# Kernel optimization log

Measured on AMD Instinct MI355X. Metric: run time of the kernel, lower is better.

Reference implementation:

```python
import jax, jax.numpy as jnp
import numpy as np

D_MODEL = 1024
N_LAYERS = 4
D_INNER = 2 * D_MODEL          # expand=2
D_STATE = 16
D_CONV = 4
DT_RANK = D_MODEL // 16        # ceil(1024/16)=64
B, T = 2, 1024


def setup_inputs() -> dict:
    key = jax.random.key(0)
    ks = jax.random.split(key, 8)
    s = 0.02
    return {
        "x": jax.random.normal(ks[0], (B, T, D_MODEL), jnp.float32),
        "in_proj_w": jax.random.normal(ks[1], (N_LAYERS, 2 * D_INNER, D_MODEL), jnp.float32) * s,
        "conv_w": jax.random.normal(ks[2], (N_LAYERS, D_INNER, D_CONV), jnp.float32) * s,
        "conv_b": jnp.zeros((N_LAYERS, D_INNER), jnp.float32),
        "x_proj_w": jax.random.normal(ks[3], (N_LAYERS, DT_RANK + 2 * D_STATE, D_INNER), jnp.float32) * s,
        "dt_proj_w": jax.random.normal(ks[4], (N_LAYERS, D_INNER, DT_RANK), jnp.float32) * s,
        "dt_proj_b": jax.random.normal(ks[5], (N_LAYERS, D_INNER), jnp.float32) * 0.1,
        "A_log": jnp.tile(jnp.log(jnp.arange(1.0, D_STATE + 1.0, dtype=jnp.float32)), (N_LAYERS, D_INNER, 1)),
        "Dd": jnp.ones((N_LAYERS, D_INNER), jnp.float32),
        "out_proj_w": jax.random.normal(ks[6], (N_LAYERS, D_MODEL, D_INNER), jnp.float32) * s,
        "norm_w": jnp.ones((D_MODEL,), jnp.float32),
        "norm_b": jnp.zeros((D_MODEL,), jnp.float32),
    }


def _silu(v):
    return v * jax.nn.sigmoid(v)


def _mamba_block(x, in_w, cw, cb, xp_w, dtp_w, dtp_b, A_log, Dv, out_w):
    # x: [B,T,d_model]
    xz = jnp.einsum('btd,ed->bte', x, in_w)            # [B,T,2*d_inner]
    u, z = jnp.split(xz, 2, axis=-1)                   # each [B,T,d_inner]
    # causal depthwise conv over time
    uc = jax.lax.conv_general_dilated(
        u.transpose(0, 2, 1),                          # [B,d_inner,T]
        cw[:, None, :],                                # [d_inner,1,K]
        window_strides=(1,), padding=[(D_CONV - 1, 0)],
        feature_group_count=D_INNER,
        dimension_numbers=('NCH', 'OIH', 'NCH'))
    uc = _silu(uc.transpose(0, 2, 1) + cb)             # [B,T,d_inner]
    x_dbl = jnp.einsum('btd,ed->bte', uc, xp_w)        # [B,T,dt_rank+2*d_state]
    dt_r = x_dbl[..., :DT_RANK]
    Bm = x_dbl[..., DT_RANK:DT_RANK + D_STATE]         # [B,T,d_state]
    Cm = x_dbl[..., DT_RANK + D_STATE:]                # [B,T,d_state]
    dt = jax.nn.softplus(jnp.einsum('btr,dr->btd', dt_r, dtp_w) + dtp_b)  # [B,T,d_inner]
    A = -jnp.exp(A_log)                                # [d_inner,d_state]

    def step(h, inp):
        u_t, dt_t, B_t, C_t = inp                      # [B,dI],[B,dI],[B,dS],[B,dS]
        h = jnp.exp(dt_t[..., None] * A) * h + (dt_t * u_t)[..., None] * B_t[:, None, :]
        return h, jnp.einsum('bds,bs->bd', h, C_t)

    h0 = jnp.zeros((x.shape[0], D_INNER, D_STATE), x.dtype)
    xs = (uc.transpose(1, 0, 2), dt.transpose(1, 0, 2), Bm.transpose(1, 0, 2), Cm.transpose(1, 0, 2))
    _, ys = jax.lax.scan(step, h0, xs)                 # ys: [T,B,d_inner]
    y = ys.transpose(1, 0, 2) + uc * Dv                # skip term D*u
    y = y * _silu(z)                                   # gated
    return jnp.einsum('btd,ed->bte', y, out_w)         # [B,T,d_model]


def reference(x, in_proj_w, conv_w, conv_b, x_proj_w, dt_proj_w, dt_proj_b, A_log, Dd, out_proj_w, norm_w, norm_b):
    for i in range(in_proj_w.shape[0]):
        residual = x
        x = _mamba_block(x, in_proj_w[i], conv_w[i], conv_b[i], x_proj_w[i],
                         dt_proj_w[i], dt_proj_b[i], A_log[i], Dd[i], out_proj_w[i])
        x = x + residual
    mu = jnp.mean(x, -1, keepdims=True)
    var = jnp.var(x, -1, keepdims=True)
    return (x - mu) / jnp.sqrt(var + 1e-5) * norm_w + norm_b
```

## Files before the change

kernel.cpp:

```cpp
#include <hip/hip_runtime.h>
#include <hip/hip_bf16.h>

#define N_LAYERS 4
#define D_MODEL  1024
#define D_INNER  2048
#define D_STATE  16
#define D_CONV   4
#define DT_RANK  64
#define BB       2
#define TT       1024
#define BT       (BB*TT)

#define NCHUNK 32
#define SCTC   (TT/NCHUNK)

#define XP_KS  8

typedef unsigned short ushort_t;
typedef __attribute__((ext_vector_type(8))) short short8;
typedef __attribute__((ext_vector_type(4))) float f32x4;

__device__ __forceinline__ float sigmoidf_(float x){ return 1.f/(1.f+__expf(-x)); }
__device__ __forceinline__ float siluf_(float x){ return x*sigmoidf_(x); }
__device__ __forceinline__ float softplusf_(float x){ return fmaxf(x,0.f) + log1pf(__expf(-fabsf(x))); }
__device__ __forceinline__ ushort_t f2b(float f){
    unsigned int x = __builtin_bit_cast(unsigned int, f);
    unsigned int r = (x + 0x7fffu + ((x>>16)&1u)) >> 16;
    return (ushort_t)r;
}
__device__ __forceinline__ float b2f(ushort_t u){
    unsigned int x = ((unsigned int)u) << 16;
    return __builtin_bit_cast(float, x);
}

#define GLOAD(g, l) __builtin_amdgcn_global_load_lds( \
    (const __attribute__((address_space(1))) void*)(g), \
    (__attribute__((address_space(3))) void*)(l), 16, 0, 0)

__global__ __launch_bounds__(256) void f2b_k(const float* __restrict__ in,
                                             ushort_t* __restrict__ out, int n){
    int i = blockIdx.x*256 + threadIdx.x;
    float4 v = ((const float4*)in)[i];
    ushort4 o;
    o.x = f2b(v.x); o.y = f2b(v.y); o.z = f2b(v.z); o.w = f2b(v.w);
    ((ushort4*)out)[i] = o;
}

__global__ __launch_bounds__(256) void f2bw_k(
    const float* __restrict__ in_w, const float* __restrict__ out_w,
    const float* __restrict__ dtp_w,
    ushort_t* __restrict__ winb, ushort_t* __restrict__ woutb,
    ushort_t* __restrict__ dtpb){
    const int n1 = (N_LAYERS*4096*1024)/4;
    const int n2 = (N_LAYERS*1024*2048)/4;
    int i = blockIdx.x*256 + threadIdx.x;
    const float4* src; ushort4* dst; int j;
    if (i < n1){ src=(const float4*)in_w;  dst=(ushort4*)winb;  j=i; }
    else if (i < n1+n2){ src=(const float4*)out_w; dst=(ushort4*)woutb; j=i-n1; }
    else { src=(const float4*)dtp_w; dst=(ushort4*)dtpb; j=i-n1-n2; }
    float4 v = src[j];
    ushort4 o;
    o.x = f2b(v.x); o.y = f2b(v.y); o.z = f2b(v.z); o.w = f2b(v.w);
    dst[j] = o;
}

__global__ __launch_bounds__(512) void gemm_ip(
    const ushort_t* __restrict__ A, const ushort_t* __restrict__ W,
    int M, int N, int K, ushort_t* __restrict__ outb,
    int RM, int RN, int XN)
{
    __shared__ ushort_t As[4][128*32];
    __shared__ ushort_t Ws[4][128*32];
    const int tid  = threadIdx.x;
    const int lane = tid & 63;
    const int wv   = tid >> 6;
    const int wm0  = (wv>>2)*64, wn0 = (wv&3)*32;

    const int bid = blockIdx.x;
    const int xcd = bid & 7, bi = bid >> 3;
    const int xm = xcd / XN, xn = xcd - xm*XN;
    const int m0 = (xm*RM + bi/RN)*128;
    const int n0 = (xn*RN + bi - (bi/RN)*RN)*128;

    const int r0 = tid>>2, ch = tid&3;

    f32x4 acc[4][2];
    #pragma unroll
    for (int i=0;i<4;++i)
        #pragma unroll
        for (int j=0;j<2;++j) acc[i][j] = (f32x4){0.f,0.f,0.f,0.f};

    const int row_a = lane & 15, kc = (lane>>4)*8;
    const ushort_t* gA = A + (size_t)(m0+r0)*K + ch*8;
    const ushort_t* gW = W + (size_t)(n0+r0)*K + ch*8;

#define STAGE(KT, BUF) { \
    GLOAD(gA + (KT)*32, (char*)&As[BUF][0] + tid*16); \
    GLOAD(gW + (KT)*32, (char*)&Ws[BUF][0] + tid*16); }

#define COMPUTE(BUF) { \
    short8 af[4], bf[2]; \
    _Pragma("unroll") \
    for (int i=0;i<4;++i) af[i] = *(const short8*)&As[BUF][(wm0 + i*16 + row_a)*32 + kc]; \
    _Pragma("unroll") \
    for (int j=0;j<2;++j) bf[j] = *(const short8*)&Ws[BUF][(wn0 + j*16 + row_a)*32 + kc]; \
    _Pragma("unroll") \
    for (int i=0;i<4;++i) \
        _Pragma("unroll") \
        for (int j=0;j<2;++j) \
            acc[i][j] = __builtin_amdgcn_mfma_f32_16x16x32_bf16(af[i], bf[j], acc[i][j], 0,0,0); }

    const int nt = K >> 5;
    STAGE(0, 0); STAGE(1, 1); STAGE(2, 2);
    for (int t = 0; t < nt-3; ++t){
        asm volatile("s_waitcnt vmcnt(4)" ::: "memory");
        asm volatile("s_barrier" ::: "memory");
        STAGE(t+3, (t+3)&3);
        COMPUTE(t&3);
    }
    asm volatile("s_waitcnt vmcnt(4)" ::: "memory");
    asm volatile("s_barrier" ::: "memory");
    COMPUTE((nt-3)&3);
    asm volatile("s_waitcnt vmcnt(2)" ::: "memory");
    asm volatile("s_barrier" ::: "memory");
    COMPUTE((nt-2)&3);
    asm volatile("s_waitcnt vmcnt(0)" ::: "memory");
    asm volatile("s_barrier" ::: "memory");
    COMPUTE((nt-1)&3);
#undef STAGE
#undef COMPUTE

    const int crow = (lane>>4)*4, ccol = lane & 15;
    #pragma unroll
    for (int i=0;i<4;++i){
        #pragma unroll
        for (int j=0;j<2;++j){
            #pragma unroll
            for (int r=0;r<4;++r){
                int m = m0 + wm0 + i*16 + crow + r;
                int n = n0 + wn0 + j*16 + ccol;
                outb[(size_t)m*N + n] = f2b(acc[i][j][r]);
            }
        }
    }
}

__global__ __launch_bounds__(256) void gemm_op(
    const ushort_t* __restrict__ A, const ushort_t* __restrict__ W,
    float* __restrict__ C, int M, int N, int K,
    const float* __restrict__ res, ushort_t* __restrict__ outb,
    int RM, int RN, int XN)
{
    __shared__ ushort_t As[4][64*32];
    __shared__ ushort_t Ws[4][64*32];
    const int tid  = threadIdx.x;
    const int lane = tid & 63;
    const int wv   = tid >> 6;
    const int wm0  = (wv>>1)*32, wn0 = (wv&1)*32;

    const int bid = blockIdx.x;
    const int xcd = bid & 7, bi = bid >> 3;
    const int xm = xcd / XN, xn = xcd - xm*XN;
    const int m0 = (xm*RM + bi/RN)*64;
    const int n0 = (xn*RN + bi - (bi/RN)*RN)*64;

    const int r0 = tid>>2, ch = tid&3;

    f32x4 acc[2][2];
    #pragma unroll
    for (int i=0;i<2;++i)
        #pragma unroll
        for (int j=0;j<2;++j) acc[i][j] = (f32x4){0.f,0.f,0.f,0.f};

    const int row_a = lane & 15, kc = (lane>>4)*8;
    const ushort_t* gA = A + (size_t)(m0+r0)*K + ch*8;
    const ushort_t* gW = W + (size_t)(n0+r0)*K + ch*8;

#define STAGE(KT, BUF) { \
    GLOAD(gA + (KT)*32, (char*)&As[BUF][0] + tid*16); \
    GLOAD(gW + (KT)*32, (char*)&Ws[BUF][0] + tid*16); }

#define COMPUTE(BUF) { \
    short8 af[2], bf[2]; \
    _Pragma("unroll") \
    for (int i=0;i<2;++i) af[i] = *(const short8*)&As[BUF][(wm0 + i*16 + row_a)*32 + kc]; \
    _Pragma("unroll") \
    for (int j=0;j<2;++j) bf[j] = *(const short8*)&Ws[BUF][(wn0 + j*16 + row_a)*32 + kc]; \
    _Pragma("unroll") \
    for (int i=0;i<2;++i) \
        _Pragma("unroll") \
        for (int j=0;j<2;++j) \
            acc[i][j] = __builtin_amdgcn_mfma_f32_16x16x32_bf16(af[i], bf[j], acc[i][j], 0,0,0); }

    const int nt = K >> 5;
    STAGE(0, 0); STAGE(1, 1); STAGE(2, 2);
    for (int t = 0; t < nt-3; ++t){
        asm volatile("s_waitcnt vmcnt(4)" ::: "memory");
        asm volatile("s_barrier" ::: "memory");
        STAGE(t+3, (t+3)&3);
        COMPUTE(t&3);
    }
    asm volatile("s_waitcnt vmcnt(4)" ::: "memory");
    asm volatile("s_barrier" ::: "memory");
    COMPUTE((nt-3)&3);
    asm volatile("s_waitcnt vmcnt(2)" ::: "memory");
    asm volatile("s_barrier" ::: "memory");
    COMPUTE((nt-2)&3);
    asm volatile("s_waitcnt vmcnt(0)" ::: "memory");
    asm volatile("s_barrier" ::: "memory");
    COMPUTE((nt-1)&3);
#undef STAGE
#undef COMPUTE

    const int crow = (lane>>4)*4, ccol = lane & 15;
    #pragma unroll
    for (int i=0;i<2;++i){
        #pragma unroll
        for (int j=0;j<2;++j){
            #pragma unroll
            for (int r=0;r<4;++r){
                int m = m0 + wm0 + i*16 + crow + r;
                int n = n0 + wn0 + j*16 + ccol;
                float v = acc[i][j][r] + res[(size_t)m*N + n];
                C[(size_t)m*N + n] = v;
                outb[(size_t)m*N + n] = f2b(v);
            }
        }
    }
}

__global__ __launch_bounds__(256) void dt_mfma(
    const ushort_t* __restrict__ A, const ushort_t* __restrict__ W,
    const float* __restrict__ bias, ushort_t* __restrict__ dtb, int N)
{
    __shared__ ushort_t As[2][64*32];
    __shared__ ushort_t Ws[2][64*32];
    const int tid = threadIdx.x, lane = tid&63, wv = tid>>6;
    const int wm0 = (wv>>1)*32, wn0 = (wv&1)*32;
    const int m0 = blockIdx.y*64, n0 = blockIdx.x*64;
    const int r0 = tid>>2, ch = tid&3;
    const ushort_t* gA = A + (size_t)(m0+r0)*64 + ch*8;
    const ushort_t* gW = W + (size_t)(n0+r0)*64 + ch*8;
    GLOAD(gA,      (char*)&As[0][0] + tid*16);
    GLOAD(gW,      (char*)&Ws[0][0] + tid*16);
    GLOAD(gA + 32, (char*)&As[1][0] + tid*16);
    GLOAD(gW + 32, (char*)&Ws[1][0] + tid*16);

    f32x4 acc[2][2];
    #pragma unroll
    for (int i=0;i<2;++i)
        #pragma unroll
        for (int j=0;j<2;++j) acc[i][j] = (f32x4){0.f,0.f,0.f,0.f};

    asm volatile("s_waitcnt vmcnt(0)" ::: "memory");
    asm volatile("s_barrier" ::: "memory");
    const int row_a = lane&15, kc = (lane>>4)*8;
    #pragma unroll
    for (int buf=0; buf<2; ++buf){
        short8 af[2], bf[2];
        #pragma unroll
        for (int i=0;i<2;++i) af[i] = *(const short8*)&As[buf][(wm0 + i*16 + row_a)*32 + kc];
        #pragma unroll
        for (int j=0;j<2;++j) bf[j] = *(const short8*)&Ws[buf][(wn0 + j*16 + row_a)*32 + kc];
        #pragma unroll
        for (int i=0;i<2;++i)
            #pragma unroll
            for (int j=0;j<2;++j)
                acc[i][j] = __builtin_amdgcn_mfma_f32_16x16x32_bf16(af[i], bf[j], acc[i][j], 0,0,0);
    }

    const int crow = (lane>>4)*4, ccol = lane & 15;
    #pragma unroll
    for (int i=0;i<2;++i){
        #pragma unroll
        for (int j=0;j<2;++j){
            #pragma unroll
            for (int r=0;r<4;++r){
                int m = m0 + wm0 + i*16 + crow + r;
                int n = n0 + wn0 + j*16 + ccol;
                float v = softplusf_(acc[i][j][r] + bias[n]);
                dtb[(size_t)m*N + n] = f2b(v);
            }
        }
    }
}

__global__ __launch_bounds__(256) void gemm_tn_sk(
    const ushort_t* __restrict__ A, int lda,
    const float* __restrict__ W, int ldw,
    float* __restrict__ P, int M, int N, int K)
{
    __shared__ float As[16][68];
    __shared__ float Ws[16][68];
    const int tid = threadIdx.x;
    const int tx = tid & 15, ty = tid >> 4;
    const int m0 = blockIdx.y * 64, n0 = blockIdx.x * 64;
    const int kbase = blockIdx.z * (K/XP_KS);
    const int lr = tid >> 2;
    const int lk = (tid & 3) << 2;
    float acc[4][4] = {{0.f}};

    for (int kk = 0; kk < K/XP_KS; kk += 16) {
        int k0 = kbase + kk;
        ushort4 av4 = *(const ushort4*)(A + (size_t)(m0+lr)*lda + k0 + lk);
        float4 wv = make_float4(0.f,0.f,0.f,0.f);
        if (n0 + lr < N) wv = *(const float4*)(W + (size_t)(n0+lr)*ldw + k0 + lk);
        __syncthreads();
        As[lk+0][lr]=b2f(av4.x); As[lk+1][lr]=b2f(av4.y);
        As[lk+2][lr]=b2f(av4.z); As[lk+3][lr]=b2f(av4.w);
        Ws[lk+0][lr]=wv.x; Ws[lk+1][lr]=wv.y; Ws[lk+2][lr]=wv.z; Ws[lk+3][lr]=wv.w;
        __syncthreads();
        #pragma unroll
        for (int k = 0; k < 16; ++k) {
            float4 a = *(const float4*)&As[k][ty<<2];
            float4 b = *(const float4*)&Ws[k][tx<<2];
            float a4[4] = {a.x,a.y,a.z,a.w};
            float b4[4] = {b.x,b.y,b.z,b.w};
            #pragma unroll
            for (int i=0;i<4;++i)
                #pragma unroll
                for (int j=0;j<4;++j)
                    acc[i][j] = fmaf(a4[i], b4[j], acc[i][j]);
        }
    }

    float* Pz = P + (size_t)blockIdx.z * M * 96;
    #pragma unroll
    for (int i=0;i<4;++i){
        int m = m0 + (ty<<2) + i;
        #pragma unroll
        for (int j=0;j<4;++j){
            int n = n0 + (tx<<2) + j;
            if (n < N) Pz[(size_t)m*96 + n] = acc[i][j];
        }
    }
}

__global__ __launch_bounds__(256) void sk_reduce(
    const float* __restrict__ P, float* __restrict__ outp,
    ushort_t* __restrict__ dtrb, int MN)
{
    int g = blockIdx.x*256 + threadIdx.x;
    float s = 0.f;
    #pragma unroll
    for (int ks=0; ks<XP_KS; ++ks) s += P[(size_t)ks*MN + g];
    outp[g] = s;
    int m = g / 96, c = g - m*96;
    if (c < 64) dtrb[(size_t)m*64 + c] = f2b(s);
}

__global__ __launch_bounds__(256) void conv_silu_k(
    const ushort_t* __restrict__ xzb, const float* __restrict__ cw,
    const float* __restrict__ cb, ushort_t* __restrict__ ucb)
{
    int idx = blockIdx.x*256 + threadIdx.x;
    int d  = idx & (D_INNER-1);
    int bt = idx >> 11;
    int t  = bt & (TT-1);
    float4 w4 = *(const float4*)(cw + d*4);
    float wv[4] = {w4.x, w4.y, w4.z, w4.w};
    float acc = cb[d];
    #pragma unroll
    for (int k=0;k<4;++k){
        int tt = t - 3 + k;
        if (tt >= 0) acc = fmaf(b2f(xzb[(size_t)(bt-3+k)*4096 + d]), wv[k], acc);
    }
    ucb[idx] = f2b(siluf_(acc));
}


__global__ __launch_bounds__(256) void scan_p1(
    const ushort_t* __restrict__ dt, const ushort_t* __restrict__ uc,
    const float* __restrict__ xdbl, const float* __restrict__ A_log,
    float* __restrict__ hpart, float* __restrict__ hdecay)
{
    const int tid = threadIdx.x;
    const int d = blockIdx.x*256 + tid;
    const int b = blockIdx.y;
    const int k = blockIdx.z;
    const int t0 = k*SCTC;
    float A[16];
    #pragma unroll
    for (int q=0;q<4;++q){
        float4 v = *(const float4*)(A_log + (size_t)d*16 + q*4);
        A[q*4+0]=-__expf(v.x); A[q*4+1]=-__expf(v.y);
        A[q*4+2]=-__expf(v.z); A[q*4+3]=-__expf(v.w);
    }
    float h[16];
    #pragma unroll
    for (int s=0;s<16;++s) h[s]=0.f;
    float sumdt = 0.f;
    const ushort_t* dtp = dt + ((size_t)b*TT + t0)*D_INNER + d;
    const ushort_t* ucp = uc + ((size_t)b*TT + t0)*D_INNER + d;
    const float* bcp = xdbl + ((size_t)b*TT + t0)*96 + 64;
    #pragma unroll 2
    for (int t=0;t<SCTC;++t){
        float dtv = b2f(dtp[(size_t)t*D_INNER]);
        float uv  = b2f(ucp[(size_t)t*D_INNER]);
        const float* bc = bcp + (size_t)t*96;
        float du = dtv*uv;
        sumdt += dtv;
        #pragma unroll
        for (int s=0;s<16;++s)
            h[s] = fmaf(__expf(dtv*A[s]), h[s], du*bc[s]);
    }
    size_t base = ((size_t)(k*BB+b)*D_INNER + d)*16;
    float4* hp = (float4*)(hpart + base);
    float4* hd = (float4*)(hdecay + base);
    #pragma unroll
    for (int q=0;q<4;++q){
        hp[q] = make_float4(h[q*4],h[q*4+1],h[q*4+2],h[q*4+3]);
        hd[q] = make_float4(__expf(sumdt*A[q*4+0]),__expf(sumdt*A[q*4+1]),
                            __expf(sumdt*A[q*4+2]),__expf(sumdt*A[q*4+3]));
    }
}

__global__ __launch_bounds__(256) void scan_fix(
    const float* __restrict__ hpart, const float* __restrict__ hdecay,
    float* __restrict__ hstart)
{
    int g = blockIdx.x*256 + threadIdx.x;
    float h = 0.f;
    #pragma unroll
    for (int k=0;k<NCHUNK;++k){
        size_t idx = (size_t)k*(BB*D_INNER*16) + g;
        hstart[idx] = h;
        h = fmaf(hdecay[idx], h, hpart[idx]);
    }
}

__global__ __launch_bounds__(256) void scan_p3(
    const ushort_t* __restrict__ dt, const ushort_t* __restrict__ uc,
    const float* __restrict__ xdbl, const float* __restrict__ A_log,
    const ushort_t* __restrict__ xzb, const float* __restrict__ Dd,
    const float* __restrict__ hstart, ushort_t* __restrict__ ysb)
{
    const int tid = threadIdx.x;
    const int d = blockIdx.x*256 + tid;
    const int b = blockIdx.y;
    const int k = blockIdx.z;
    const int t0 = k*SCTC;
    float A[16];
    #pragma unroll
    for (int q=0;q<4;++q){
        float4 v = *(const float4*)(A_log + (size_t)d*16 + q*4);
        A[q*4+0]=-__expf(v.x); A[q*4+1]=-__expf(v.y);
        A[q*4+2]=-__expf(v.z); A[q*4+3]=-__expf(v.w);
    }
    float h[16];
    {
        const float4* hs = (const float4*)(hstart + ((size_t)(k*BB+b)*D_INNER + d)*16);
        #pragma unroll
        for (int q=0;q<4;++q){
            float4 v = hs[q];
            h[q*4+0]=v.x; h[q*4+1]=v.y; h[q*4+2]=v.z; h[q*4+3]=v.w;
        }
    }
    const float Ddc = Dd[d];
    const ushort_t* dtp = dt + ((size_t)b*TT + t0)*D_INNER + d;
    const ushort_t* ucp = uc + ((size_t)b*TT + t0)*D_INNER + d;
    const ushort_t* zp = xzb + ((size_t)b*TT + t0)*4096 + 2048 + d;
    const float* bcp = xdbl + ((size_t)b*TT + t0)*96 + 64;
    ushort_t* yp = ysb + ((size_t)b*TT + t0)*D_INNER + d;
    #pragma unroll 2
    for (int t=0;t<SCTC;++t){
        float dtv = b2f(dtp[(size_t)t*D_INNER]);
        float uv  = b2f(ucp[(size_t)t*D_INNER]);
        float zv  = b2f(zp[(size_t)t*4096]);
        const float* bc = bcp + (size_t)t*96;
        float du = dtv*uv;
        float y0=0.f,y1=0.f,y2=0.f,y3=0.f;
        #pragma unroll
        for (int q=0;q<4;++q){
            h[q*4+0] = fmaf(__expf(dtv*A[q*4+0]), h[q*4+0], du*bc[q*4+0]);
            h[q*4+1] = fmaf(__expf(dtv*A[q*4+1]), h[q*4+1], du*bc[q*4+1]);
            h[q*4+2] = fmaf(__expf(dtv*A[q*4+2]), h[q*4+2], du*bc[q*4+2]);
            h[q*4+3] = fmaf(__expf(dtv*A[q*4+3]), h[q*4+3], du*bc[q*4+3]);
        }
        #pragma unroll
        for (int q=0;q<4;++q){
            y0 = fmaf(h[q*4+0], bc[16+q*4+0], y0);
            y1 = fmaf(h[q*4+1], bc[16+q*4+1], y1);
            y2 = fmaf(h[q*4+2], bc[16+q*4+2], y2);
            y3 = fmaf(h[q*4+3], bc[16+q*4+3], y3);
        }
        float y = (y0+y1)+(y2+y3);
        float yv = (y + uv*Ddc) * siluf_(zv);
        yp[(size_t)t*D_INNER] = f2b(yv);
    }
}

__global__ __launch_bounds__(256) void layernorm_k(
    const float* __restrict__ X, const float* __restrict__ w,
    const float* __restrict__ b, float* __restrict__ out)
{
    int row = blockIdx.x;
    int tid = threadIdx.x;
    const float* xr = X + (size_t)row*D_MODEL;
    float4 v = *(const float4*)(xr + tid*4);
    float s  = v.x+v.y+v.z+v.w;
    float ss = fmaf(v.x,v.x, fmaf(v.y,v.y, fmaf(v.z,v.z, v.w*v.w)));
    #pragma unroll
    for (int off=32; off>0; off>>=1){
        s  += __shfl_down(s, off, 64);
        ss += __shfl_down(ss, off, 64);
    }
    __shared__ float red[8];
    int wid = tid>>6, lane = tid&63;
    if (lane==0){ red[wid]=s; red[4+wid]=ss; }
    __syncthreads();
    if (tid==0){
        float S  = red[0]+red[1]+red[2]+red[3];
        float SS = red[4]+red[5]+red[6]+red[7];
        float mu = S*(1.f/D_MODEL);
        float var = SS*(1.f/D_MODEL) - mu*mu;
        red[0]=mu; red[1]=rsqrtf(var + 1e-5f);
    }
    __syncthreads();
    float mu=red[0], rs=red[1];
    float4 wv = *(const float4*)(w + tid*4);
    float4 bv = *(const float4*)(b + tid*4);
    float4 o;
    o.x = fmaf((v.x-mu)*rs, wv.x, bv.x);
    o.y = fmaf((v.y-mu)*rs, wv.y, bv.y);
    o.z = fmaf((v.z-mu)*rs, wv.z, bv.z);
    o.w = fmaf((v.w-mu)*rs, wv.w, bv.w);
    *(float4*)(out + (size_t)row*D_MODEL + tid*4) = o;
}

extern "C" void kernel_launch(void* const* d_in, const int* in_sizes, int n_in,
                              void* d_out, int out_size, void* d_ws, size_t ws_size,
                              hipStream_t stream) {
    (void)in_sizes; (void)n_in; (void)out_size; (void)ws_size;
    const float* x      = (const float*)d_in[0];
    const float* in_w   = (const float*)d_in[1];
    const float* conv_w = (const float*)d_in[2];
    const float* conv_b = (const float*)d_in[3];
    const float* xp_w   = (const float*)d_in[4];
    const float* dtp_w  = (const float*)d_in[5];
    const float* dtp_b  = (const float*)d_in[6];
    const float* A_log  = (const float*)d_in[7];
    const float* Dd     = (const float*)d_in[8];
    const float* out_w  = (const float*)d_in[9];
    const float* nw     = (const float*)d_in[10];
    const float* nb     = (const float*)d_in[11];
    float* out = (float*)d_out;

    char* p = (char*)d_ws;
    ushort_t* xzb  = (ushort_t*)p; p += (size_t)BT*4096*2;
    ushort_t* ucb  = (ushort_t*)p; p += (size_t)BT*2048*2;
    float* xdbl    = (float*)p;  p += (size_t)BT*96*4;
    ushort_t* dtrb = (ushort_t*)p; p += (size_t)BT*64*2;
    ushort_t* dtbb = (ushort_t*)p; p += (size_t)BT*2048*2;
    float* xcur    = (float*)p;  p += (size_t)BT*1024*4;
    ushort_t* xinb = (ushort_t*)p; p += (size_t)BT*1024*2;
    ushort_t* ysb  = (ushort_t*)p; p += (size_t)BT*2048*2;
    ushort_t* winb = (ushort_t*)p; p += (size_t)N_LAYERS*4096*1024*2;
    ushort_t* woutb= (ushort_t*)p; p += (size_t)N_LAYERS*1024*2048*2;
    ushort_t* dtpb = (ushort_t*)p; p += (size_t)N_LAYERS*2048*64*2;
    float* hpart   = (float*)p;  p += (size_t)NCHUNK*BB*D_INNER*16*4;
    float* hdecay  = (float*)p;  p += (size_t)NCHUNK*BB*D_INNER*16*4;
    float* hstart  = (float*)p;  p += (size_t)NCHUNK*BB*D_INNER*16*4;
    float* pbuf    = hpart;

    f2b_k<<<(BT*1024)/1024,256,0,stream>>>(x, xinb, BT*1024);
    f2bw_k<<<(N_LAYERS*(4096*1024 + 1024*2048 + 2048*64))/1024,256,0,stream>>>(
        in_w, out_w, dtp_w, winb, woutb, dtpb);

    for (int i = 0; i < N_LAYERS; ++i){
        const float* xin = (i==0) ? x : xcur;
        gemm_ip<<<512,512,0,stream>>>(
            xinb, winb + (size_t)i*4096*1024, BT, 4096, D_MODEL, xzb, 8, 8, 4);
        conv_silu_k<<<(BT*D_INNER)/256,256,0,stream>>>(
            xzb, conv_w + (size_t)i*D_INNER*D_CONV, conv_b + (size_t)i*D_INNER, ucb);
        gemm_tn_sk<<<dim3(2,32,XP_KS),256,0,stream>>>(
            ucb, D_INNER, xp_w + (size_t)i*96*D_INNER, D_INNER,
            pbuf, BT, 96, D_INNER);
        sk_reduce<<<(BT*96)/256,256,0,stream>>>(pbuf, xdbl, dtrb, BT*96);
        dt_mfma<<<dim3(D_INNER/64, BT/64),256,0,stream>>>(
            dtrb, dtpb + (size_t)i*2048*64, dtp_b + (size_t)i*D_INNER, dtbb, D_INNER);
        scan_p1<<<dim3(D_INNER/256, BB, NCHUNK),256,0,stream>>>(
            dtbb, ucb, xdbl, A_log + (size_t)i*D_INNER*D_STATE, hpart, hdecay);
        scan_fix<<<(BB*D_INNER*16)/256,256,0,stream>>>(hpart, hdecay, hstart);
        scan_p3<<<dim3(D_INNER/256, BB, NCHUNK),256,0,stream>>>(
            dtbb, ucb, xdbl, A_log + (size_t)i*D_INNER*D_STATE, xzb,
            Dd + (size_t)i*D_INNER, hstart, ysb);
        gemm_op<<<512,256,0,stream>>>(
            ysb, woutb + (size_t)i*1024*2048, xcur, BT, 1024, D_INNER,
            xin, xinb, 8, 8, 2);
    }
    layernorm_k<<<BT,256,0,stream>>>(xcur, nw, nb, out);
}
```

Before: 681.6 us.

## Fuse conv+SiLU into consumers, merge cast kernels, deepen out-proj pipeline, add setprio

Removes the standalone conv_silu kernel and its ucb buffer. The causal depthwise conv and SiLU are now recomputed inside the x_proj split-K GEMM and both scan passes, reading the u half of xzb directly. The separate input and weight bf16 cast kernels are merged into one launch. The out-proj GEMM stages two K-tiles per barrier across six LDS buffers, and s_setprio is raised around the MFMA sections. Together these cut launches and an intermediate round trip through memory, at the cost of redundant conv math, more LDS use and more register pressure.

```diff
diff --git a/kernel.cpp b/kernel.cpp
--- a/kernel.cpp
+++ b/kernel.cpp
@@ -37,27 +37,21 @@
     (const __attribute__((address_space(1))) void*)(g), \
     (__attribute__((address_space(3))) void*)(l), 16, 0, 0)
 
-__global__ __launch_bounds__(256) void f2b_k(const float* __restrict__ in,
-                                             ushort_t* __restrict__ out, int n){
-    int i = blockIdx.x*256 + threadIdx.x;
-    float4 v = ((const float4*)in)[i];
-    ushort4 o;
-    o.x = f2b(v.x); o.y = f2b(v.y); o.z = f2b(v.z); o.w = f2b(v.w);
-    ((ushort4*)out)[i] = o;
-}
-
-__global__ __launch_bounds__(256) void f2bw_k(
-    const float* __restrict__ in_w, const float* __restrict__ out_w,
-    const float* __restrict__ dtp_w,
-    ushort_t* __restrict__ winb, ushort_t* __restrict__ woutb,
-    ushort_t* __restrict__ dtpb){
+__global__ __launch_bounds__(256) void f2ball_k(
+    const float* __restrict__ x, const float* __restrict__ in_w,
+    const float* __restrict__ out_w, const float* __restrict__ dtp_w,
+    ushort_t* __restrict__ xinb, ushort_t* __restrict__ winb,
+    ushort_t* __restrict__ woutb, ushort_t* __restrict__ dtpb)
+{
+    const int n0 = (BT*1024)/4;
     const int n1 = (N_LAYERS*4096*1024)/4;
     const int n2 = (N_LAYERS*1024*2048)/4;
     int i = blockIdx.x*256 + threadIdx.x;
     const float4* src; ushort4* dst; int j;
-    if (i < n1){ src=(const float4*)in_w;  dst=(ushort4*)winb;  j=i; }
-    else if (i < n1+n2){ src=(const float4*)out_w; dst=(ushort4*)woutb; j=i-n1; }
-    else { src=(const float4*)dtp_w; dst=(ushort4*)dtpb; j=i-n1-n2; }
+    if (i < n0){ src=(const float4*)x; dst=(ushort4*)xinb; j=i; }
+    else if (i < n0+n1){ src=(const float4*)in_w; dst=(ushort4*)winb; j=i-n0; }
+    else if (i < n0+n1+n2){ src=(const float4*)out_w; dst=(ushort4*)woutb; j=i-n0-n1; }
+    else { src=(const float4*)dtp_w; dst=(ushort4*)dtpb; j=i-n0-n1-n2; }
     float4 v = src[j];
     ushort4 o;
     o.x = f2b(v.x); o.y = f2b(v.y); o.z = f2b(v.z); o.w = f2b(v.w);
@@ -104,11 +98,13 @@
     for (int i=0;i<4;++i) af[i] = *(const short8*)&As[BUF][(wm0 + i*16 + row_a)*32 + kc]; \
     _Pragma("unroll") \
     for (int j=0;j<2;++j) bf[j] = *(const short8*)&Ws[BUF][(wn0 + j*16 + row_a)*32 + kc]; \
+    __builtin_amdgcn_s_setprio(1); \
     _Pragma("unroll") \
     for (int i=0;i<4;++i) \
         _Pragma("unroll") \
         for (int j=0;j<2;++j) \
-            acc[i][j] = __builtin_amdgcn_mfma_f32_16x16x32_bf16(af[i], bf[j], acc[i][j], 0,0,0); }
+            acc[i][j] = __builtin_amdgcn_mfma_f32_16x16x32_bf16(af[i], bf[j], acc[i][j], 0,0,0); \
+    __builtin_amdgcn_s_setprio(0); }
 
     const int nt = K >> 5;
     STAGE(0, 0); STAGE(1, 1); STAGE(2, 2);
@@ -151,8 +147,8 @@
     const float* __restrict__ res, ushort_t* __restrict__ outb,
     int RM, int RN, int XN)
 {
-    __shared__ ushort_t As[4][64*32];
-    __shared__ ushort_t Ws[4][64*32];
+    __shared__ ushort_t As[6][64*32];
+    __shared__ ushort_t Ws[6][64*32];
     const int tid  = threadIdx.x;
     const int lane = tid & 63;
     const int wv   = tid >> 6;
@@ -192,23 +188,30 @@
         for (int j=0;j<2;++j) \
             acc[i][j] = __builtin_amdgcn_mfma_f32_16x16x32_bf16(af[i], bf[j], acc[i][j], 0,0,0); }
 
-    const int nt = K >> 5;
-    STAGE(0, 0); STAGE(1, 1); STAGE(2, 2);
-    for (int t = 0; t < nt-3; ++t){
+    const int np = K >> 6;
+    STAGE(0, 0); STAGE(1, 1);
+    STAGE(2, 2); STAGE(3, 3);
+    for (int p = 0; p < np-2; ++p){
+        const int bA = (p%3)*2, bS = ((p+2)%3)*2;
         asm volatile("s_waitcnt vmcnt(4)" ::: "memory");
         asm volatile("s_barrier" ::: "memory");
-        STAGE(t+3, (t+3)&3);
-        COMPUTE(t&3);
-    }
-    asm volatile("s_waitcnt vmcnt(4)" ::: "memory");
-    asm volatile("s_barrier" ::: "memory");
-    COMPUTE((nt-3)&3);
-    asm volatile("s_waitcnt vmcnt(2)" ::: "memory");
-    asm volatile("s_barrier" ::: "memory");
-    COMPUTE((nt-2)&3);
-    asm volatile("s_waitcnt vmcnt(0)" ::: "memory");
-    asm volatile("s_barrier" ::: "memory");
-    COMPUTE((nt-1)&3);
+        STAGE(2*p+4, bS); STAGE(2*p+5, bS+1);
+        __builtin_amdgcn_s_setprio(1);
+        COMPUTE(bA); COMPUTE(bA+1);
+        __builtin_amdgcn_s_setprio(0);
+    }
+    {
+        const int bA = ((np-2)%3)*2;
+        asm volatile("s_waitcnt vmcnt(4)" ::: "memory");
+        asm volatile("s_barrier" ::: "memory");
+        COMPUTE(bA); COMPUTE(bA+1);
+    }
+    {
+        const int bA = ((np-1)%3)*2;
+        asm volatile("s_waitcnt vmcnt(0)" ::: "memory");
+        asm volatile("s_barrier" ::: "memory");
+        COMPUTE(bA); COMPUTE(bA+1);
+    }
 #undef STAGE
 #undef COMPUTE
 
@@ -286,7 +289,8 @@
 }
 
 __global__ __launch_bounds__(256) void gemm_tn_sk(
-    const ushort_t* __restrict__ A, int lda,
+    const ushort_t* __restrict__ xzb, const float* __restrict__ cw,
+    const float* __restrict__ cb,
     const float* __restrict__ W, int ldw,
     float* __restrict__ P, int M, int N, int K)
 {
@@ -299,16 +303,37 @@
     const int lr = tid >> 2;
     const int lk = (tid & 3) << 2;
     float acc[4][4] = {{0.f}};
+    const int m = m0 + lr;
+    const int t = m & (TT-1);
 
     for (int kk = 0; kk < K/XP_KS; kk += 16) {
-        int k0 = kbase + kk;
-        ushort4 av4 = *(const ushort4*)(A + (size_t)(m0+lr)*lda + k0 + lk);
-        float4 wv = make_float4(0.f,0.f,0.f,0.f);
-        if (n0 + lr < N) wv = *(const float4*)(W + (size_t)(n0+lr)*ldw + k0 + lk);
+        const int k0 = kbase + kk;
+        const int colb = k0 + lk;
+        ushort4 z4; z4.x=0; z4.y=0; z4.z=0; z4.w=0;
+        ushort4 xr0 = (t >= 3) ? *(const ushort4*)(xzb + (size_t)(m-3)*4096 + colb) : z4;
+        ushort4 xr1 = (t >= 2) ? *(const ushort4*)(xzb + (size_t)(m-2)*4096 + colb) : z4;
+        ushort4 xr2 = (t >= 1) ? *(const ushort4*)(xzb + (size_t)(m-1)*4096 + colb) : z4;
+        ushort4 xr3 = *(const ushort4*)(xzb + (size_t)m*4096 + colb);
+        const ushort_t* q0 = (const ushort_t*)&xr0;
+        const ushort_t* q1 = (const ushort_t*)&xr1;
+        const ushort_t* q2 = (const ushort_t*)&xr2;
+        const ushort_t* q3 = (const ushort_t*)&xr3;
+        float av[4];
+        #pragma unroll
+        for (int jj=0;jj<4;++jj){
+            float4 w4 = *(const float4*)(cw + (size_t)(colb+jj)*4);
+            float a = cb[colb+jj];
+            a = fmaf(b2f(q0[jj]), w4.x, a);
+            a = fmaf(b2f(q1[jj]), w4.y, a);
+            a = fmaf(b2f(q2[jj]), w4.z, a);
+            a = fmaf(b2f(q3[jj]), w4.w, a);
+            av[jj] = siluf_(a);
+        }
+        float4 wvv = make_float4(0.f,0.f,0.f,0.f);
+        if (n0 + lr < N) wvv = *(const float4*)(W + (size_t)(n0+lr)*ldw + k0 + lk);
         __syncthreads();
-        As[lk+0][lr]=b2f(av4.x); As[lk+1][lr]=b2f(av4.y);
-        As[lk+2][lr]=b2f(av4.z); As[lk+3][lr]=b2f(av4.w);
-        Ws[lk+0][lr]=wv.x; Ws[lk+1][lr]=wv.y; Ws[lk+2][lr]=wv.z; Ws[lk+3][lr]=wv.w;
+        As[lk+0][lr]=av[0]; As[lk+1][lr]=av[1]; As[lk+2][lr]=av[2]; As[lk+3][lr]=av[3];
+        Ws[lk+0][lr]=wvv.x; Ws[lk+1][lr]=wvv.y; Ws[lk+2][lr]=wvv.z; Ws[lk+3][lr]=wvv.w;
         __syncthreads();
         #pragma unroll
         for (int k = 0; k < 16; ++k) {
@@ -327,11 +352,11 @@
     float* Pz = P + (size_t)blockIdx.z * M * 96;
     #pragma unroll
     for (int i=0;i<4;++i){
-        int m = m0 + (ty<<2) + i;
+        int mm = m0 + (ty<<2) + i;
         #pragma unroll
         for (int j=0;j<4;++j){
             int n = n0 + (tx<<2) + j;
-            if (n < N) Pz[(size_t)m*96 + n] = acc[i][j];
+            if (n < N) Pz[(size_t)mm*96 + n] = acc[i][j];
         }
     }
 }
@@ -349,28 +374,10 @@
     if (c < 64) dtrb[(size_t)m*64 + c] = f2b(s);
 }
 
-__global__ __launch_bounds__(256) void conv_silu_k(
-    const ushort_t* __restrict__ xzb, const float* __restrict__ cw,
-    const float* __restrict__ cb, ushort_t* __restrict__ ucb)
-{
-    int idx = blockIdx.x*256 + threadIdx.x;
-    int d  = idx & (D_INNER-1);
-    int bt = idx >> 11;
-    int t  = bt & (TT-1);
-    float4 w4 = *(const float4*)(cw + d*4);
-    float wv[4] = {w4.x, w4.y, w4.z, w4.w};
-    float acc = cb[d];
-    #pragma unroll
-    for (int k=0;k<4;++k){
-        int tt = t - 3 + k;
-        if (tt >= 0) acc = fmaf(b2f(xzb[(size_t)(bt-3+k)*4096 + d]), wv[k], acc);
-    }
-    ucb[idx] = f2b(siluf_(acc));
-}
-
 
 __global__ __launch_bounds__(256) void scan_p1(
-    const ushort_t* __restrict__ dt, const ushort_t* __restrict__ uc,
+    const ushort_t* __restrict__ dt, const ushort_t* __restrict__ xzb,
+    const float* __restrict__ cw, const float* __restrict__ cb,
     const float* __restrict__ xdbl, const float* __restrict__ A_log,
     float* __restrict__ hpart, float* __restrict__ hdecay)
 {
@@ -391,12 +398,22 @@
     for (int s=0;s<16;++s) h[s]=0.f;
     float sumdt = 0.f;
     const ushort_t* dtp = dt + ((size_t)b*TT + t0)*D_INNER + d;
-    const ushort_t* ucp = uc + ((size_t)b*TT + t0)*D_INNER + d;
+    const ushort_t* up  = xzb + ((size_t)b*TT + t0)*4096 + d;
     const float* bcp = xdbl + ((size_t)b*TT + t0)*96 + 64;
+    float4 w4 = *(const float4*)(cw + (size_t)d*4);
+    const float cbd = cb[d];
+    float u3=0.f, u2=0.f, u1=0.f;
+    if (t0 > 0){
+        u3 = b2f(*(up - 3*4096));
+        u2 = b2f(*(up - 2*4096));
+        u1 = b2f(*(up - 4096));
+    }
     #pragma unroll 2
     for (int t=0;t<SCTC;++t){
         float dtv = b2f(dtp[(size_t)t*D_INNER]);
-        float uv  = b2f(ucp[(size_t)t*D_INNER]);
+        float u0  = b2f(up[(size_t)t*4096]);
+        float uv = siluf_(fmaf(u0,w4.w, fmaf(u1,w4.z, fmaf(u2,w4.y, fmaf(u3,w4.x, cbd)))));
+        u3=u2; u2=u1; u1=u0;
         const float* bc = bcp + (size_t)t*96;
         float du = dtv*uv;
         sumdt += dtv;
@@ -430,10 +447,11 @@
 }
 
 __global__ __launch_bounds__(256) void scan_p3(
-    const ushort_t* __restrict__ dt, const ushort_t* __restrict__ uc,
+    const ushort_t* __restrict__ dt, const ushort_t* __restrict__ xzb,
+    const float* __restrict__ cw, const float* __restrict__ cb,
     const float* __restrict__ xdbl, const float* __restrict__ A_log,
-    const ushort_t* __restrict__ xzb, const float* __restrict__ Dd,
-    const float* __restrict__ hstart, ushort_t* __restrict__ ysb)
+    const float* __restrict__ Dd, const float* __restrict__ hstart,
+    ushort_t* __restrict__ ysb)
 {
     const int tid = threadIdx.x;
     const int d = blockIdx.x*256 + tid;
@@ -458,14 +476,24 @@
     }
     const float Ddc = Dd[d];
     const ushort_t* dtp = dt + ((size_t)b*TT + t0)*D_INNER + d;
-    const ushort_t* ucp = uc + ((size_t)b*TT + t0)*D_INNER + d;
-    const ushort_t* zp = xzb + ((size_t)b*TT + t0)*4096 + 2048 + d;
+    const ushort_t* up  = xzb + ((size_t)b*TT + t0)*4096 + d;
+    const ushort_t* zp  = xzb + ((size_t)b*TT + t0)*4096 + 2048 + d;
     const float* bcp = xdbl + ((size_t)b*TT + t0)*96 + 64;
     ushort_t* yp = ysb + ((size_t)b*TT + t0)*D_INNER + d;
+    float4 w4 = *(const float4*)(cw + (size_t)d*4);
+    const float cbd = cb[d];
+    float u3=0.f, u2=0.f, u1=0.f;
+    if (t0 > 0){
+        u3 = b2f(*(up - 3*4096));
+        u2 = b2f(*(up - 2*4096));
+        u1 = b2f(*(up - 4096));
+    }
     #pragma unroll 2
     for (int t=0;t<SCTC;++t){
         float dtv = b2f(dtp[(size_t)t*D_INNER]);
-        float uv  = b2f(ucp[(size_t)t*D_INNER]);
+        float u0  = b2f(up[(size_t)t*4096]);
+        float uv = siluf_(fmaf(u0,w4.w, fmaf(u1,w4.z, fmaf(u2,w4.y, fmaf(u3,w4.x, cbd)))));
+        u3=u2; u2=u1; u1=u0;
         float zv  = b2f(zp[(size_t)t*4096]);
         const float* bc = bcp + (size_t)t*96;
         float du = dtv*uv;
@@ -548,7 +576,6 @@
 
     char* p = (char*)d_ws;
     ushort_t* xzb  = (ushort_t*)p; p += (size_t)BT*4096*2;
-    ushort_t* ucb  = (ushort_t*)p; p += (size_t)BT*2048*2;
     float* xdbl    = (float*)p;  p += (size_t)BT*96*4;
     ushort_t* dtrb = (ushort_t*)p; p += (size_t)BT*64*2;
     ushort_t* dtbb = (ushort_t*)p; p += (size_t)BT*2048*2;
@@ -563,27 +590,27 @@
     float* hstart  = (float*)p;  p += (size_t)NCHUNK*BB*D_INNER*16*4;
     float* pbuf    = hpart;
 
-    f2b_k<<<(BT*1024)/1024,256,0,stream>>>(x, xinb, BT*1024);
-    f2bw_k<<<(N_LAYERS*(4096*1024 + 1024*2048 + 2048*64))/1024,256,0,stream>>>(
-        in_w, out_w, dtp_w, winb, woutb, dtpb);
+    f2ball_k<<<(BT*1024 + N_LAYERS*(4096*1024 + 1024*2048 + 2048*64))/1024,
+               256,0,stream>>>(x, in_w, out_w, dtp_w, xinb, winb, woutb, dtpb);
 
     for (int i = 0; i < N_LAYERS; ++i){
         const float* xin = (i==0) ? x : xcur;
+        const float* cw = conv_w + (size_t)i*D_INNER*D_CONV;
+        const float* cb = conv_b + (size_t)i*D_INNER;
         gemm_ip<<<512,512,0,stream>>>(
             xinb, winb + (size_t)i*4096*1024, BT, 4096, D_MODEL, xzb, 8, 8, 4);
-        conv_silu_k<<<(BT*D_INNER)/256,256,0,stream>>>(
-            xzb, conv_w + (size_t)i*D_INNER*D_CONV, conv_b + (size_t)i*D_INNER, ucb);
         gemm_tn_sk<<<dim3(2,32,XP_KS),256,0,stream>>>(
-            ucb, D_INNER, xp_w + (size_t)i*96*D_INNER, D_INNER,
+            xzb, cw, cb, xp_w + (size_t)i*96*D_INNER, D_INNER,
             pbuf, BT, 96, D_INNER);
         sk_reduce<<<(BT*96)/256,256,0,stream>>>(pbuf, xdbl, dtrb, BT*96);
         dt_mfma<<<dim3(D_INNER/64, BT/64),256,0,stream>>>(
             dtrb, dtpb + (size_t)i*2048*64, dtp_b + (size_t)i*D_INNER, dtbb, D_INNER);
         scan_p1<<<dim3(D_INNER/256, BB, NCHUNK),256,0,stream>>>(
-            dtbb, ucb, xdbl, A_log + (size_t)i*D_INNER*D_STATE, hpart, hdecay);
+            dtbb, xzb, cw, cb, xdbl, A_log + (size_t)i*D_INNER*D_STATE,
+            hpart, hdecay);
         scan_fix<<<(BB*D_INNER*16)/256,256,0,stream>>>(hpart, hdecay, hstart);
         scan_p3<<<dim3(D_INNER/256, BB, NCHUNK),256,0,stream>>>(
-            dtbb, ucb, xdbl, A_log + (size_t)i*D_INNER*D_STATE, xzb,
+            dtbb, xzb, cw, cb, xdbl, A_log + (size_t)i*D_INNER*D_STATE,
             Dd + (size_t)i*D_INNER, hstart, ysb);
         gemm_op<<<512,256,0,stream>>>(
             ysb, woutb + (size_t)i*1024*2048, xcur, BT, 1024, D_INNER,
```

Result: slower. 718.2 us (+5.4%).
